# Kernel optimization log

Measured on AMD Instinct MI355X. Metric: run time of the kernel, lower is better.

The kernel has to match this reference:

```python
import jax, jax.numpy as jnp
import numpy as np

B, H, S, D = 1, 16, 4096, 64


def setup_inputs() -> dict:
    key = jax.random.key(0)
    kq, kk, kv = jax.random.split(key, 3)
    Q = jax.random.normal(kq, (B, H, S, D), dtype=jnp.float32)
    K = jax.random.normal(kk, (B, H, S, D), dtype=jnp.float32)
    V = jax.random.normal(kv, (B, H, S, D), dtype=jnp.float32)
    # causal mask, broadcast over batch/heads: True = attend
    mask = jnp.tril(jnp.ones((S, S), dtype=bool))[None, None, :, :]
    return {"Q": Q, "K": K, "V": V, "mask": mask}


def reference(Q, K, V, mask):
    d_k = Q.shape[-1]
    scale = 1.0 / jnp.sqrt(jnp.asarray(d_k, dtype=Q.dtype))
    # [..., q, k] scores; mask==False positions set to -inf before softmax
    scores = jnp.einsum('...qd,...kd->...qk', Q, K) * scale
    scores = jnp.where(mask, scores, jnp.asarray(-jnp.inf, dtype=scores.dtype))
    attn = jax.nn.softmax(scores, axis=-1)
    return jnp.einsum('...qk,...kd->...qd', attn, V)
```

## Files before the change

### kernel.cpp

```cpp
#include <hip/hip_runtime.h>
#include <hip/hip_bf16.h>

typedef __attribute__((ext_vector_type(8))) short short8;
typedef __attribute__((ext_vector_type(4))) short s4v;
typedef __attribute__((ext_vector_type(4))) float floatx4;
typedef __attribute__((ext_vector_type(4))) float float4v;

#define MFMA16(A,B,C) __builtin_amdgcn_mfma_f32_16x16x32_bf16(A,B,C,0,0,0)

__device__ __forceinline__ short bf16bits(float x) {
    __hip_bfloat16 h = __float2bfloat16(x);
    return *(short*)&h;
}
__device__ __forceinline__ short8 cvt8(const float* p) {
    float4v a = *(const float4v*)p;
    float4v b = *(const float4v*)(p + 4);
    short8 r;
    r[0]=bf16bits(a.x); r[1]=bf16bits(a.y); r[2]=bf16bits(a.z); r[3]=bf16bits(a.w);
    r[4]=bf16bits(b.x); r[5]=bf16bits(b.y); r[6]=bf16bits(b.z); r[7]=bf16bits(b.w);
    return r;
}

__global__ __launch_bounds__(256) void kcvt(const float* __restrict__ K,
                                            short* __restrict__ K16) {
    const size_t i = ((size_t)blockIdx.x * 256 + threadIdx.x) * 8;
    *(short8*)(K16 + i) = cvt8(K + i);
}

__global__ __launch_bounds__(256) void vtrans(const float* __restrict__ V,
                                              short* __restrict__ VT) {
    __shared__ short tile[64 * 65];
    const int t  = threadIdx.x;
    const int h  = blockIdx.x >> 6;
    const int s0 = (blockIdx.x & 63) << 6;
    const float* src = V + ((size_t)h * 4096 + s0) * 64;
    const int r  = t >> 4;
    const int dq = (t & 15) * 4;
#pragma unroll
    for (int pass = 0; pass < 4; ++pass) {
        const int s = pass * 16 + r;
        float4v f = *(const float4v*)(src + s * 64 + dq);
        short* w = tile + s * 65 + dq;
        w[0] = bf16bits(f.x); w[1] = bf16bits(f.y);
        w[2] = bf16bits(f.z); w[3] = bf16bits(f.w);
    }
    __syncthreads();
    const int d  = t >> 2;
    const int sc = (t & 3) * 16;
    short8 a, b;
#pragma unroll
    for (int j = 0; j < 8; ++j) a[j] = tile[(sc + j) * 65 + d];
#pragma unroll
    for (int j = 0; j < 8; ++j) b[j] = tile[(sc + 8 + j) * 65 + d];
    short* dst = VT + ((size_t)h * 64 + d) * 4096 + s0 + sc;
    *(short8*)dst       = a;
    *(short8*)(dst + 8) = b;
}

template<bool KB16>
__global__ __launch_bounds__(256, 4)
void attn_fast(const float* __restrict__ Qg, const float* __restrict__ Kg,
               const short* __restrict__ K16g, const short* __restrict__ VTg,
               float* __restrict__ Og)
{
    constexpr int S = 4096, D = 64;
    constexpr float SCL2 = 0.125f * 1.44269504088896f;
    constexpr float MSUB = 20.0f;

    __shared__ __align__(16) short lK[2048];
    __shared__ __align__(16) short lV[2048];
    __shared__ __align__(16) short lP[2048];

    const int tid = threadIdx.x;
    const int wv  = tid >> 6;
    const int ln  = tid & 63;
    const int ll  = ln & 15;
    const int qd  = ln >> 4;

    const int c = blockIdx.x & 255;
    const int s = blockIdx.x >> 8;
    const int h = c & 15;
    const int x = c >> 4;
    const int qblk = (s == 0) ? (63 - x) : (s == 1) ? (32 + x) : (s == 2) ? (31 - x) : x;
    const int qb   = qblk << 6;
    const int qrow = qb + wv * 16;

    const float* Qh  = Qg  + (size_t)h * S * D;
    const float* Kf  = Kg  + (size_t)h * S * D;
    const short* K16 = K16g + (size_t)h * S * D;
    const short* Vt  = VTg + (size_t)h * 64 * S;

    short8 qf0, qf1;
    {
        const float* qp = Qh + (qrow + ll) * D + qd * 8;
        qf0 = cvt8(qp);
        qf1 = cvt8(qp + 32);
    }

    floatx4 o[4], ol;
#pragma unroll
    for (int dt = 0; dt < 4; ++dt) o[dt] = (floatx4){0.f, 0.f, 0.f, 0.f};
    ol = (floatx4){0.f, 0.f, 0.f, 0.f};

    short8 ones;
#pragma unroll
    for (int j = 0; j < 8; ++j) ones[j] = (short)0x3F80;

    const int kkey = tid >> 3, kd8 = tid & 7;
    const int koct = kd8 & 3;
    short* kdst = lK + ((kkey >> 4) * 2 + (kd8 >> 2)) * 512
                     + ((((kkey & 15) | (koct << 4)) ^ (koct * 5)) * 8);
    const float* ksrcf = Kf  + kkey * 64 + kd8 * 8;
    const short* ksrc6 = K16 + kkey * 64 + kd8 * 8;
    const int vd = tid >> 2, voct = tid & 3;
    short* vdst = lV + (vd >> 4) * 512
                     + ((((vd & 15) | (voct << 4)) ^ (voct * 5)) * 8);
    const short* vsrc = Vt + (size_t)vd * S + voct * 8;
    const int rblk = ((ll | (qd << 4)) ^ (qd * 5));
    const int pswz  = (ll >> 1) & 3;
    short* lPw = lP + wv * 512;
    const int pw0 = ll * 32 + (((qd >> 1) ^ pswz) * 8) + (qd & 1) * 4;
    const int prd = ll * 32 + ((qd ^ pswz) * 8);

    const int kv_end = qb + 64;
    const int wv_end = qrow + 16;

    auto ldK = [&](int kv) -> short8 {
        return KB16 ? *(const short8*)(ksrc6 + kv * 64) : cvt8(ksrcf + kv * 64);
    };

    short8 kpre = ldK(0);
    short8 vpre = *(const short8*)(vsrc);

    for (int kv = 0; kv < kv_end; kv += 32) {
        __syncthreads();
        *(short8*)kdst = kpre;
        *(short8*)vdst = vpre;
        __syncthreads();
        if (kv + 32 < kv_end) {
            kpre = ldK(kv + 32);
            vpre = *(const short8*)(vsrc + kv + 32);
        }

        if (kv < wv_end) {
            floatx4 sc0 = (floatx4){0.f, 0.f, 0.f, 0.f};
            floatx4 sc1 = sc0;
            short8 kf;
            kf = ((const short8*)(lK +    0))[rblk]; sc0 = MFMA16(kf, qf0, sc0);
            kf = ((const short8*)(lK +  512))[rblk]; sc0 = MFMA16(kf, qf1, sc0);
            kf = ((const short8*)(lK + 1024))[rblk]; sc1 = MFMA16(kf, qf0, sc1);
            kf = ((const short8*)(lK + 1536))[rblk]; sc1 = MFMA16(kf, qf1, sc1);

            float p0[4], p1[4];
#pragma unroll
            for (int r = 0; r < 4; ++r) {
                p0[r] = exp2f(fmaf(sc0[r], SCL2, -MSUB));
                p1[r] = exp2f(fmaf(sc1[r], SCL2, -MSUB));
            }
            if (kv + 31 > qrow) {
                const int qg = qrow + ll;
                const int k0 = kv + qd * 4, k1 = k0 + 16;
#pragma unroll
                for (int r = 0; r < 4; ++r) {
                    if (k0 + r > qg) p0[r] = 0.f;
                    if (k1 + r > qg) p1[r] = 0.f;
                }
            }
            s4v w0, w1;
#pragma unroll
            for (int r = 0; r < 4; ++r) { w0[r] = bf16bits(p0[r]); w1[r] = bf16bits(p1[r]); }
            *(s4v*)(lPw + pw0)        = w0;
            *(s4v*)(lPw + (pw0 ^ 16)) = w1;
            __threadfence_block();
            short8 pf = *(const short8*)(lPw + prd);
#pragma unroll
            for (int dt = 0; dt < 4; ++dt) {
                short8 vf = ((const short8*)(lV + dt * 512))[rblk];
                o[dt] = MFMA16(pf, vf, o[dt]);
            }
            ol = MFMA16(pf, ones, ol);
        }
    }

#pragma unroll
    for (int r = 0; r < 4; ++r) {
        const float rl = 1.f / fmaxf(ol[r], 1e-37f);
        const int q = qrow + qd * 4 + r;
        float* op = Og + ((size_t)h * S + q) * D + ll;
#pragma unroll
        for (int dt = 0; dt < 4; ++dt)
            op[dt * 16] = o[dt][r] * rl;
    }
}

__global__ __launch_bounds__(256, 4)
void attn_legacy(const float* __restrict__ Qg, const float* __restrict__ Kg,
                 const float* __restrict__ Vg, float* __restrict__ Og)
{
    constexpr int S = 4096, D = 64;
    constexpr float SCL2 = 0.125f * 1.44269504088896f;
    constexpr float NEG  = -1.0e30f;
    __shared__ __align__(16) short lK[2048];
    __shared__ __align__(16) short lV[2048];
    __shared__ __align__(16) short lP[2048];
    const int tid = threadIdx.x, wv = tid >> 6, ln = tid & 63, ll = ln & 15, qd = ln >> 4;
    const int bid = blockIdx.x, h = bid & 15, qblk = 63 - (bid >> 4), qb = qblk << 6;
    const float* Qh = Qg + (size_t)h * S * D;
    const float* Kh = Kg + (size_t)h * S * D;
    const float* Vh = Vg + (size_t)h * S * D;
    const int qrow = qb + wv * 16;
    short8 qf0, qf1;
    { const float* qp = Qh + (qrow + ll) * D + qd * 8; qf0 = cvt8(qp); qf1 = cvt8(qp + 32); }
    floatx4 o[4]; float mi[4], li[4];
#pragma unroll
    for (int dt = 0; dt < 4; ++dt) o[dt] = (floatx4){0.f,0.f,0.f,0.f};
#pragma unroll
    for (int r = 0; r < 4; ++r) { mi[r] = NEG; li[r] = 0.f; }
    const int k_st = tid >> 3, dbase = (tid & 7) * 8;
    const int sq = (dbase >> 3) & 3, sks = dbase >> 5;
    const int kw_slot = (((k_st >> 4) * 2 + sks) * 64)
                      + (((sq << 4) | (k_st & 15)) ^ (sq | (sks << 2)));
    const int kr0 = ln ^ qd, kr1 = ln ^ (qd | 4), vbit3 = (ln >> 3) & 1;
    const int kv_end = qb + 64, wv_end = qrow + 16;
    for (int kv = 0; kv < kv_end; kv += 32) {
        __syncthreads();
        {
            short8 kval = cvt8(Kh + (kv + k_st) * D + dbase);
            ((short8*)lK)[kw_slot] = kval;
            short8 vval = cvt8(Vh + (kv + k_st) * D + dbase);
            const int vq = (k_st >> 3) << 4, vj = k_st & 7;
#pragma unroll
            for (int i = 0; i < 8; ++i) {
                int d = dbase + i, dt = d >> 4, l2 = d & 15;
                int lp = (vq | l2) ^ (((l2 >> 3) & 1) | (dt << 1));
                lV[dt * 512 + lp * 8 + vj] = vval[i];
            }
        }
        __syncthreads();
        if (kv < wv_end) {
            floatx4 sc0 = (floatx4){0.f,0.f,0.f,0.f}, sc1 = sc0; short8 kf;
            kf = ((const short8*)lK)[0*64+kr0]; sc0 = MFMA16(qf0, kf, sc0);
            kf = ((const short8*)lK)[1*64+kr1]; sc0 = MFMA16(qf1, kf, sc0);
            kf = ((const short8*)lK)[2*64+kr0]; sc1 = MFMA16(qf0, kf, sc1);
            kf = ((const short8*)lK)[3*64+kr1]; sc1 = MFMA16(qf1, kf, sc1);
            float p0[4], p1[4]; const int qg = qrow + qd * 4;
#pragma unroll
            for (int r = 0; r < 4; ++r) { p0[r] = sc0[r]*SCL2; p1[r] = sc1[r]*SCL2; }
            if (kv + 31 > qrow) {
                const int k0 = kv + ll, k1 = kv + 16 + ll;
#pragma unroll
                for (int r = 0; r < 4; ++r) {
                    if (k0 > qg + r) p0[r] = NEG;
                    if (k1 > qg + r) p1[r] = NEG;
                }
            }
#pragma unroll
            for (int r = 0; r < 4; ++r) {
                float mx = fmaxf(p0[r], p1[r]);
                mx = fmaxf(mx, __shfl_xor(mx,1)); mx = fmaxf(mx, __shfl_xor(mx,2));
                mx = fmaxf(mx, __shfl_xor(mx,4)); mx = fmaxf(mx, __shfl_xor(mx,8));
                const float nm = fmaxf(mi[r], mx);
                const float a = exp2f(mi[r] - nm); mi[r] = nm;
                p0[r] = exp2f(p0[r] - nm); p1[r] = exp2f(p1[r] - nm);
                float ps = p0[r] + p1[r];
                ps += __shfl_xor(ps,1); ps += __shfl_xor(ps,2);
                ps += __shfl_xor(ps,4); ps += __shfl_xor(ps,8);
                li[r] = li[r] * a + ps;
#pragma unroll
                for (int dt = 0; dt < 4; ++dt) o[dt][r] *= a;
            }
            {
                const int pbase = wv * 512 + (ll & 7);
                const int dl0 = ((ll >> 3) << 4) + qd * 4;
#pragma unroll
                for (int r = 0; r < 4; ++r) {
                    lP[pbase + (dl0 + r) * 8]      = bf16bits(p0[r]);
                    lP[pbase + (dl0 + 32 + r) * 8] = bf16bits(p1[r]);
                }
            }
            __threadfence_block();
            short8 pf = ((const short8*)lP)[wv * 64 + ln];
#pragma unroll
            for (int dt = 0; dt < 4; ++dt) {
                short8 vf = ((const short8*)lV)[dt * 64 + (ln ^ (vbit3 | (dt << 1)))];
                o[dt] = MFMA16(pf, vf, o[dt]);
            }
        }
    }
#pragma unroll
    for (int r = 0; r < 4; ++r) {
        const float rl = 1.f / fmaxf(li[r], 1e-30f);
        const int q = qrow + qd * 4 + r;
        float* op = Og + ((size_t)h * S + q) * D + ll;
#pragma unroll
        for (int dt = 0; dt < 4; ++dt) op[dt * 16] = o[dt][r] * rl;
    }
}

extern "C" void kernel_launch(void* const* d_in, const int* in_sizes, int n_in,
                              void* d_out, int out_size, void* d_ws, size_t ws_size,
                              hipStream_t stream) {
    const float* Q = (const float*)d_in[0];
    const float* K = (const float*)d_in[1];
    const float* V = (const float*)d_in[2];
    float* O = (float*)d_out;
    const size_t elems = (size_t)16 * 4096 * 64;
    const size_t oneBuf = elems * sizeof(short);
    if (ws_size >= 2 * oneBuf) {
        short* VT  = (short*)d_ws;
        short* K16 = (short*)d_ws + elems;
        vtrans<<<dim3(16 * 64), dim3(256), 0, stream>>>(V, VT);
        kcvt<<<dim3(elems / (256 * 8)), dim3(256), 0, stream>>>(K, K16);
        attn_fast<true><<<dim3(1024), dim3(256), 0, stream>>>(Q, K, K16, VT, O);
    } else if (ws_size >= oneBuf) {
        short* VT = (short*)d_ws;
        vtrans<<<dim3(16 * 64), dim3(256), 0, stream>>>(V, VT);
        attn_fast<false><<<dim3(1024), dim3(256), 0, stream>>>(Q, K, nullptr, VT, O);
    } else {
        attn_legacy<<<dim3(1024), dim3(256), 0, stream>>>(Q, K, V, O);
    }
}
```

Measured before the change: 208.1 us.

## Enlarge attention tiles to 128 queries and 64 keys, fuse prep kernels

Each block now handles 128 query rows, with every wave covering 32 rows as two 16-row subtiles. Each iteration stages 64 keys, so every K/V fragment read from LDS feeds two query subtiles and there are half as many barrier iterations. Fully masked 16-key subblocks skip their MFMAs and write zero probabilities. The V transpose and the K bf16 conversion are merged into one prep kernel to save a launch. In exchange there are fewer blocks (512), larger LDS use and more registers, with launch bounds lowered to 2 blocks per CU, so occupancy and load balance across CUs may drop.

```diff
diff --git a/kernel.cpp b/kernel.cpp
--- a/kernel.cpp
+++ b/kernel.cpp
@@ -4,7 +4,6 @@
 typedef __attribute__((ext_vector_type(8))) short short8;
 typedef __attribute__((ext_vector_type(4))) short s4v;
 typedef __attribute__((ext_vector_type(4))) float floatx4;
-typedef __attribute__((ext_vector_type(4))) float float4v;
 
 #define MFMA16(A,B,C) __builtin_amdgcn_mfma_f32_16x16x32_bf16(A,B,C,0,0,0)
 
@@ -13,40 +12,35 @@
     return *(short*)&h;
 }
 __device__ __forceinline__ short8 cvt8(const float* p) {
-    float4v a = *(const float4v*)p;
-    float4v b = *(const float4v*)(p + 4);
+    floatx4 a = *(const floatx4*)p;
+    floatx4 b = *(const floatx4*)(p + 4);
     short8 r;
     r[0]=bf16bits(a.x); r[1]=bf16bits(a.y); r[2]=bf16bits(a.z); r[3]=bf16bits(a.w);
     r[4]=bf16bits(b.x); r[5]=bf16bits(b.y); r[6]=bf16bits(b.z); r[7]=bf16bits(b.w);
     return r;
 }
 
-__global__ __launch_bounds__(256) void kcvt(const float* __restrict__ K,
-                                            short* __restrict__ K16) {
-    const size_t i = ((size_t)blockIdx.x * 256 + threadIdx.x) * 8;
-    *(short8*)(K16 + i) = cvt8(K + i);
-}
-
-__global__ __launch_bounds__(256) void vtrans(const float* __restrict__ V,
-                                              short* __restrict__ VT) {
+__global__ __launch_bounds__(256) void prep(const float* __restrict__ V,
+                                            short* __restrict__ VT,
+                                            const float* __restrict__ K,
+                                            short* __restrict__ K16, int doK)
+{
     __shared__ short tile[64 * 65];
     const int t  = threadIdx.x;
     const int h  = blockIdx.x >> 6;
     const int s0 = (blockIdx.x & 63) << 6;
     const float* src = V + ((size_t)h * 4096 + s0) * 64;
-    const int r  = t >> 4;
-    const int dq = (t & 15) * 4;
+    const int r = t >> 4, dq = (t & 15) * 4;
 #pragma unroll
     for (int pass = 0; pass < 4; ++pass) {
         const int s = pass * 16 + r;
-        float4v f = *(const float4v*)(src + s * 64 + dq);
+        floatx4 f = *(const floatx4*)(src + s * 64 + dq);
         short* w = tile + s * 65 + dq;
         w[0] = bf16bits(f.x); w[1] = bf16bits(f.y);
         w[2] = bf16bits(f.z); w[3] = bf16bits(f.w);
     }
     __syncthreads();
-    const int d  = t >> 2;
-    const int sc = (t & 3) * 16;
+    const int d = t >> 2, sc = (t & 3) * 16;
     short8 a, b;
 #pragma unroll
     for (int j = 0; j < 8; ++j) a[j] = tile[(sc + j) * 65 + d];
@@ -55,10 +49,15 @@
     short* dst = VT + ((size_t)h * 64 + d) * 4096 + s0 + sc;
     *(short8*)dst       = a;
     *(short8*)(dst + 8) = b;
+    if (doK) {
+        const size_t base = (size_t)blockIdx.x * 4096 + (size_t)t * 16;
+        *(short8*)(K16 + base)     = cvt8(K + base);
+        *(short8*)(K16 + base + 8) = cvt8(K + base + 8);
+    }
 }
 
 template<bool KB16>
-__global__ __launch_bounds__(256, 4)
+__global__ __launch_bounds__(256, 2)
 void attn_fast(const float* __restrict__ Qg, const float* __restrict__ Kg,
                const short* __restrict__ K16g, const short* __restrict__ VTg,
                float* __restrict__ Og)
@@ -67,9 +66,9 @@
     constexpr float SCL2 = 0.125f * 1.44269504088896f;
     constexpr float MSUB = 20.0f;
 
-    __shared__ __align__(16) short lK[2048];
-    __shared__ __align__(16) short lV[2048];
-    __shared__ __align__(16) short lP[2048];
+    __shared__ __align__(16) short lK[4096];
+    __shared__ __align__(16) short lV[4096];
+    __shared__ __align__(16) short lP[8192];
 
     const int tid = threadIdx.x;
     const int wv  = tid >> 6;
@@ -77,119 +76,141 @@
     const int ll  = ln & 15;
     const int qd  = ln >> 4;
 
-    const int c = blockIdx.x & 255;
-    const int s = blockIdx.x >> 8;
-    const int h = c & 15;
-    const int x = c >> 4;
-    const int qblk = (s == 0) ? (63 - x) : (s == 1) ? (32 + x) : (s == 2) ? (31 - x) : x;
-    const int qb   = qblk << 6;
-    const int qrow = qb + wv * 16;
+    const int bid = blockIdx.x;
+    const int c   = bid & 255;
+    const int h   = c & 15;
+    const int x   = c >> 4;
+    const int qblk = (bid >> 8) ? x : (31 - x);
+    const int qb   = qblk << 7;
+    const int qrow0 = qb + wv * 32;
 
     const float* Qh  = Qg  + (size_t)h * S * D;
     const float* Kf  = Kg  + (size_t)h * S * D;
     const short* K16 = K16g + (size_t)h * S * D;
     const short* Vt  = VTg + (size_t)h * 64 * S;
 
-    short8 qf0, qf1;
-    {
-        const float* qp = Qh + (qrow + ll) * D + qd * 8;
-        qf0 = cvt8(qp);
-        qf1 = cvt8(qp + 32);
-    }
-
-    floatx4 o[4], ol;
-#pragma unroll
-    for (int dt = 0; dt < 4; ++dt) o[dt] = (floatx4){0.f, 0.f, 0.f, 0.f};
-    ol = (floatx4){0.f, 0.f, 0.f, 0.f};
-
+    short8 qf[2][2];
+#pragma unroll
+    for (int qs = 0; qs < 2; ++qs) {
+        const float* qp = Qh + (size_t)(qrow0 + qs * 16 + ll) * D + qd * 8;
+        qf[qs][0] = cvt8(qp);
+        qf[qs][1] = cvt8(qp + 32);
+    }
+
+    floatx4 o[2][4], ol[2];
+#pragma unroll
+    for (int qs = 0; qs < 2; ++qs) {
+        ol[qs] = (floatx4){0.f, 0.f, 0.f, 0.f};
+#pragma unroll
+        for (int dt = 0; dt < 4; ++dt) o[qs][dt] = (floatx4){0.f, 0.f, 0.f, 0.f};
+    }
     short8 ones;
 #pragma unroll
     for (int j = 0; j < 8; ++j) ones[j] = (short)0x3F80;
 
-    const int kkey = tid >> 3, kd8 = tid & 7;
-    const int koct = kd8 & 3;
-    short* kdst = lK + ((kkey >> 4) * 2 + (kd8 >> 2)) * 512
-                     + ((((kkey & 15) | (koct << 4)) ^ (koct * 5)) * 8);
-    const float* ksrcf = Kf  + kkey * 64 + kd8 * 8;
-    const short* ksrc6 = K16 + kkey * 64 + kd8 * 8;
+    const int key0 = tid >> 3, kd8 = tid & 7;
+    const int koctS = kd8 & 3;
+    short* kdst = lK + ((key0 >> 4) * 2 + (kd8 >> 2)) * 512
+                     + ((((key0 & 15) | (koctS << 4)) ^ (koctS * 5)) * 8);
+    const short* ks6 = K16 + key0 * 64 + kd8 * 8;
+    const float* ksf = Kf  + key0 * 64 + kd8 * 8;
     const int vd = tid >> 2, voct = tid & 3;
-    short* vdst = lV + (vd >> 4) * 512
+    short* vdst = lV + ((vd >> 4) * 2) * 512
                      + ((((vd & 15) | (voct << 4)) ^ (voct * 5)) * 8);
-    const short* vsrc = Vt + (size_t)vd * S + voct * 8;
-    const int rblk = ((ll | (qd << 4)) ^ (qd * 5));
-    const int pswz  = (ll >> 1) & 3;
-    short* lPw = lP + wv * 512;
-    const int pw0 = ll * 32 + (((qd >> 1) ^ pswz) * 8) + (qd & 1) * 4;
-    const int prd = ll * 32 + ((qd ^ pswz) * 8);
-
-    const int kv_end = qb + 64;
-    const int wv_end = qrow + 16;
-
-    auto ldK = [&](int kv) -> short8 {
-        return KB16 ? *(const short8*)(ksrc6 + kv * 64) : cvt8(ksrcf + kv * 64);
+    const short* vs = Vt + (size_t)vd * S + voct * 8;
+
+    const int rblk8 = (((ll | (qd << 4)) ^ (qd * 5))) * 8;
+    short* lPw = lP + wv * 2048;
+    const int pkoct_h = qd >> 1;
+    const int pj = (qd & 1) * 4;
+
+    const int kv_end  = qb + 128;
+    const int wv_lim  = qrow0 + 32;
+
+    auto ldK = [&](int kv, int pass) -> short8 {
+        return KB16 ? *(const short8*)(ks6 + kv * 64 + pass * 2048)
+                    : cvt8(ksf + kv * 64 + pass * 2048);
     };
 
-    short8 kpre = ldK(0);
-    short8 vpre = *(const short8*)(vsrc);
-
-    for (int kv = 0; kv < kv_end; kv += 32) {
+    short8 kpre0 = ldK(0, 0), kpre1 = ldK(0, 1);
+    short8 vpre0 = *(const short8*)(vs);
+    short8 vpre1 = *(const short8*)(vs + 32);
+
+    for (int kv = 0; kv < kv_end; kv += 64) {
         __syncthreads();
-        *(short8*)kdst = kpre;
-        *(short8*)vdst = vpre;
+        *(short8*)kdst          = kpre0;
+        *(short8*)(kdst + 2048) = kpre1;
+        *(short8*)vdst          = vpre0;
+        *(short8*)(vdst + 512)  = vpre1;
         __syncthreads();
-        if (kv + 32 < kv_end) {
-            kpre = ldK(kv + 32);
-            vpre = *(const short8*)(vsrc + kv + 32);
-        }
-
-        if (kv < wv_end) {
-            floatx4 sc0 = (floatx4){0.f, 0.f, 0.f, 0.f};
-            floatx4 sc1 = sc0;
-            short8 kf;
-            kf = ((const short8*)(lK +    0))[rblk]; sc0 = MFMA16(kf, qf0, sc0);
-            kf = ((const short8*)(lK +  512))[rblk]; sc0 = MFMA16(kf, qf1, sc0);
-            kf = ((const short8*)(lK + 1024))[rblk]; sc1 = MFMA16(kf, qf0, sc1);
-            kf = ((const short8*)(lK + 1536))[rblk]; sc1 = MFMA16(kf, qf1, sc1);
-
-            float p0[4], p1[4];
-#pragma unroll
-            for (int r = 0; r < 4; ++r) {
-                p0[r] = exp2f(fmaf(sc0[r], SCL2, -MSUB));
-                p1[r] = exp2f(fmaf(sc1[r], SCL2, -MSUB));
-            }
-            if (kv + 31 > qrow) {
-                const int qg = qrow + ll;
-                const int k0 = kv + qd * 4, k1 = k0 + 16;
-#pragma unroll
-                for (int r = 0; r < 4; ++r) {
-                    if (k0 + r > qg) p0[r] = 0.f;
-                    if (k1 + r > qg) p1[r] = 0.f;
+        if (kv + 64 < kv_end) {
+            kpre0 = ldK(kv + 64, 0);
+            kpre1 = ldK(kv + 64, 1);
+            vpre0 = *(const short8*)(vs + kv + 64);
+            vpre1 = *(const short8*)(vs + kv + 96);
+        }
+        if (kv >= wv_lim) continue;
+
+#pragma unroll
+        for (int kb = 0; kb < 4; ++kb) {
+            short8 kf0 = *(const short8*)(lK + (kb * 2 + 0) * 512 + rblk8);
+            short8 kf1 = *(const short8*)(lK + (kb * 2 + 1) * 512 + rblk8);
+            const int kbase = kv + kb * 16;
+            const int koct  = (kb & 1) * 2 + pkoct_h;
+            const int poff  = (((ll | (koct << 4)) ^ (koct * 5))) * 8 + pj;
+#pragma unroll
+            for (int qs = 0; qs < 2; ++qs) {
+                short* pw = lPw + (qs * 2 + (kb >> 1)) * 512 + poff;
+                const int qsrow = qrow0 + qs * 16;
+                if (kbase > qsrow + 15) {
+                    *(s4v*)pw = (s4v){0, 0, 0, 0};
+                } else {
+                    floatx4 sc = MFMA16(kf0, qf[qs][0], ((floatx4){0.f,0.f,0.f,0.f}));
+                    sc = MFMA16(kf1, qf[qs][1], sc);
+                    float p[4];
+#pragma unroll
+                    for (int r = 0; r < 4; ++r)
+                        p[r] = exp2f(fmaf(sc[r], SCL2, -MSUB));
+                    if (kbase + 15 > qsrow) {
+                        const int qg = qsrow + ll;
+                        const int k0 = kbase + qd * 4;
+#pragma unroll
+                        for (int r = 0; r < 4; ++r)
+                            if (k0 + r > qg) p[r] = 0.f;
+                    }
+                    s4v w;
+#pragma unroll
+                    for (int r = 0; r < 4; ++r) w[r] = bf16bits(p[r]);
+                    *(s4v*)pw = w;
                 }
             }
-            s4v w0, w1;
-#pragma unroll
-            for (int r = 0; r < 4; ++r) { w0[r] = bf16bits(p0[r]); w1[r] = bf16bits(p1[r]); }
-            *(s4v*)(lPw + pw0)        = w0;
-            *(s4v*)(lPw + (pw0 ^ 16)) = w1;
-            __threadfence_block();
-            short8 pf = *(const short8*)(lPw + prd);
+        }
+        __threadfence_block();
+#pragma unroll
+        for (int kh = 0; kh < 2; ++kh) {
+            short8 pf0 = *(const short8*)(lPw + (0 + kh) * 512 + rblk8);
+            short8 pf1 = *(const short8*)(lPw + (2 + kh) * 512 + rblk8);
 #pragma unroll
             for (int dt = 0; dt < 4; ++dt) {
-                short8 vf = ((const short8*)(lV + dt * 512))[rblk];
-                o[dt] = MFMA16(pf, vf, o[dt]);
-            }
-            ol = MFMA16(pf, ones, ol);
-        }
-    }
-
+                short8 vf = *(const short8*)(lV + (dt * 2 + kh) * 512 + rblk8);
+                o[0][dt] = MFMA16(pf0, vf, o[0][dt]);
+                o[1][dt] = MFMA16(pf1, vf, o[1][dt]);
+            }
+            ol[0] = MFMA16(pf0, ones, ol[0]);
+            ol[1] = MFMA16(pf1, ones, ol[1]);
+        }
+    }
+
+#pragma unroll
+    for (int qs = 0; qs < 2; ++qs)
 #pragma unroll
     for (int r = 0; r < 4; ++r) {
-        const float rl = 1.f / fmaxf(ol[r], 1e-37f);
-        const int q = qrow + qd * 4 + r;
+        const float rl = 1.f / fmaxf(ol[qs][r], 1e-37f);
+        const int q = qrow0 + qs * 16 + qd * 4 + r;
         float* op = Og + ((size_t)h * S + q) * D + ll;
 #pragma unroll
         for (int dt = 0; dt < 4; ++dt)
-            op[dt * 16] = o[dt][r] * rl;
+            op[dt * 16] = o[qs][dt][r] * rl;
     }
 }
 
@@ -304,18 +325,17 @@
     const float* K = (const float*)d_in[1];
     const float* V = (const float*)d_in[2];
     float* O = (float*)d_out;
-    const size_t elems = (size_t)16 * 4096 * 64;
+    const size_t elems  = (size_t)16 * 4096 * 64;
     const size_t oneBuf = elems * sizeof(short);
     if (ws_size >= 2 * oneBuf) {
         short* VT  = (short*)d_ws;
         short* K16 = (short*)d_ws + elems;
-        vtrans<<<dim3(16 * 64), dim3(256), 0, stream>>>(V, VT);
-        kcvt<<<dim3(elems / (256 * 8)), dim3(256), 0, stream>>>(K, K16);
-        attn_fast<true><<<dim3(1024), dim3(256), 0, stream>>>(Q, K, K16, VT, O);
+        prep<<<dim3(1024), dim3(256), 0, stream>>>(V, VT, K, K16, 1);
+        attn_fast<true><<<dim3(512), dim3(256), 0, stream>>>(Q, K, K16, VT, O);
     } else if (ws_size >= oneBuf) {
         short* VT = (short*)d_ws;
-        vtrans<<<dim3(16 * 64), dim3(256), 0, stream>>>(V, VT);
-        attn_fast<false><<<dim3(1024), dim3(256), 0, stream>>>(Q, K, nullptr, VT, O);
+        prep<<<dim3(1024), dim3(256), 0, stream>>>(V, VT, K, VT, 0);
+        attn_fast<false><<<dim3(512), dim3(256), 0, stream>>>(Q, K, nullptr, VT, O);
     } else {
         attn_legacy<<<dim3(1024), dim3(256), 0, stream>>>(Q, K, V, O);
     }
```

New measurement: 244.7 us. 17.6% more time.
